# Optimization experiments

Measured on AMD Instinct MI355X. Metric: run time of the kernel, lower is better.

The kernel has to match this reference:

```python
import jax, jax.numpy as jnp
import numpy as np

D = 2048      # hidden
H = 16        # heads
HD = 128      # head dim
E = 64        # experts
K = 8         # top-k
F = 1024      # expert intermediate
B, S = 1, 256
EPS = 1e-05
THETA = 10000.0
SCALE = 0.08838834764831845  # 1/sqrt(128)


def _rms(x, w):
    return x * jax.lax.rsqrt(jnp.mean(x * x, axis=-1, keepdims=True) + EPS) * w


def _rotate_half(x):
    h = x.shape[-1] // 2
    return jnp.concatenate([-x[..., h:], x[..., :h]], axis=-1)


def setup_inputs() -> dict:
    key = jax.random.key(0)
    ks = jax.random.split(key, 16)
    std = 0.02
    return {
        "x": jax.random.normal(ks[0], (B, S, D), jnp.float32),
        "ln1_w": jnp.ones((D,), jnp.float32),
        "q_w": jax.random.normal(ks[1], (D, D), jnp.float32) * std,
        "k_w": jax.random.normal(ks[2], (D, D), jnp.float32) * std,
        "v_w": jax.random.normal(ks[3], (D, D), jnp.float32) * std,
        "o_w": jax.random.normal(ks[4], (D, D), jnp.float32) * std,
        "qn_w": jnp.ones((D,), jnp.float32),
        "kn_w": jnp.ones((D,), jnp.float32),
        "ln2_w": jnp.ones((D,), jnp.float32),
        "router_w": jax.random.normal(ks[5], (E, D), jnp.float32) * std,
        "gate_w": jax.random.normal(ks[6], (E, F, D), jnp.float32) * std,
        "up_w": jax.random.normal(ks[7], (E, F, D), jnp.float32) * std,
        "down_w": jax.random.normal(ks[8], (E, D, F), jnp.float32) * std,
    }


def reference(x, ln1_w, q_w, k_w, v_w, o_w, qn_w, kn_w, ln2_w,
              router_w, gate_w, up_w, down_w):
    b, s, d = x.shape
    # ---- attention ----
    xn = _rms(x, ln1_w)
    q = _rms(jnp.einsum('bsd,od->bso', xn, q_w), qn_w)
    k = _rms(jnp.einsum('bsd,od->bso', xn, k_w), kn_w)
    v = jnp.einsum('bsd,od->bso', xn, v_w)
    q = q.reshape(b, s, H, HD).transpose(0, 2, 1, 3)  # [b,h,s,hd]
    k = k.reshape(b, s, H, HD).transpose(0, 2, 1, 3)
    v = v.reshape(b, s, H, HD).transpose(0, 2, 1, 3)
    # RoPE
    inv_freq = 1.0 / (THETA ** (jnp.arange(0, HD, 2, dtype=jnp.float32) / HD))
    ang = jnp.arange(s, dtype=jnp.float32)[:, None] * inv_freq[None, :]  # [s, hd/2]
    emb = jnp.concatenate([ang, ang], axis=-1)
    cos, sin = jnp.cos(emb).astype(x.dtype), jnp.sin(emb).astype(x.dtype)
    q = q * cos + _rotate_half(q) * sin
    k = k * cos + _rotate_half(k) * sin
    scores = jnp.einsum('bhqd,bhkd->bhqk', q, k) * SCALE
    causal = jnp.tril(jnp.ones((s, s), bool))
    scores = jnp.where(causal, scores, jnp.finfo(scores.dtype).min)
    attn = jax.nn.softmax(scores, axis=-1)
    ctx = jnp.einsum('bhqk,bhkd->bhqd', attn, v)
    ctx = ctx.transpose(0, 2, 1, 3).reshape(b, s, d)
    h = x + jnp.einsum('bsd,od->bso', ctx, o_w)
    # ---- MoE ----
    hn = _rms(h, ln2_w)
    logits = jnp.einsum('bsd,ed->bse', hn, router_w)
    probs = jax.nn.softmax(logits.astype(jnp.float32), axis=-1)
    vals, idx = jax.lax.top_k(probs, K)  # [b,s,K]
    # dense combine weights [b,s,E]; OLMoE does not renormalize top-k probs
    combine = jnp.sum(jax.nn.one_hot(idx, E, dtype=jnp.float32) * vals[..., None], axis=-2)
    combine = combine.reshape(-1, E).astype(x.dtype)  # [T,E]
    xf = hn.reshape(-1, d)                            # [T,D]
    g = jnp.einsum('td,efd->etf', xf, gate_w)         # [E,T,F]
    u = jnp.einsum('td,efd->etf', xf, up_w)
    mid = jax.nn.silu(g) * u
    eo = jnp.einsum('etf,edf->etd', mid, down_w)      # [E,T,D]
    y = jnp.einsum('te,etd->td', combine, eo).reshape(b, s, d)
    return h + y
```

## Files before the change

### kernel.cpp

```cpp
#include <hip/hip_runtime.h>
#include <math.h>

#define DHID 2048
#define TOK 256
#define NHEAD 16
#define HDIM 128
#define NEXP 64
#define KSEL 8
#define FFD 1024
#define RMSEPS 1e-5f
#define ATTNSCALE 0.08838834764831845f

typedef short bf16x8 __attribute__((ext_vector_type(8)));
typedef float f32x4 __attribute__((ext_vector_type(4)));
typedef float f4 __attribute__((ext_vector_type(4)));

__device__ __forceinline__ unsigned short f2bf(float f){
  union { float f; unsigned int u; } c; c.f = f;
  unsigned int u = c.u + 0x7fffu + ((c.u>>16)&1u);
  return (unsigned short)(u>>16);
}
__device__ __forceinline__ unsigned int pk2(float a, float b){
  return (unsigned int)f2bf(a) | ((unsigned int)f2bf(b)<<16);
}
__device__ __forceinline__ bf16x8 as_bf8(uint4 u){
  union { uint4 u; bf16x8 v; } c; c.u = u; return c.v;
}

#define WAITV(N) { asm volatile("s_waitcnt vmcnt(" #N ")" ::: "memory"); __builtin_amdgcn_sched_barrier(0); }
#define WAITL0   { asm volatile("s_waitcnt lgkmcnt(0)" ::: "memory"); __builtin_amdgcn_sched_barrier(0); }
#define SB       __builtin_amdgcn_sched_barrier(0);

__global__ __launch_bounds__(256) void rms_kernel(const float* __restrict__ x,
    const float* __restrict__ w, unsigned short* __restrict__ obf,
    float* __restrict__ of32)
{
  int row = blockIdx.x, tid = threadIdx.x;
  const float* xr = x + (size_t)row*DHID;
  float4 a = *(const float4*)(xr + tid*8);
  float4 b = *(const float4*)(xr + tid*8 + 4);
  float ss = a.x*a.x+a.y*a.y+a.z*a.z+a.w*a.w + b.x*b.x+b.y*b.y+b.z*b.z+b.w*b.w;
  #pragma unroll
  for(int o=32;o>0;o>>=1) ss += __shfl_down(ss,o);
  __shared__ float red[4];
  if((tid&63)==0) red[tid>>6]=ss;
  __syncthreads();
  float r = rsqrtf((red[0]+red[1]+red[2]+red[3])*(1.0f/DHID) + RMSEPS);
  float v[8] = {a.x,a.y,a.z,a.w,b.x,b.y,b.z,b.w};
  unsigned short ob[8];
  #pragma unroll
  for(int j=0;j<8;j++){
    float val = v[j]*r*w[tid*8+j];
    ob[j]=f2bf(val);
    if(of32) of32[(size_t)row*DHID + tid*8 + j] = val;
  }
  uint4 o4;
  o4.x = (unsigned int)ob[0] | ((unsigned int)ob[1]<<16);
  o4.y = (unsigned int)ob[2] | ((unsigned int)ob[3]<<16);
  o4.z = (unsigned int)ob[4] | ((unsigned int)ob[5]<<16);
  o4.w = (unsigned int)ob[6] | ((unsigned int)ob[7]<<16);
  *(uint4*)(obf + (size_t)row*DHID + tid*8) = o4;
}

__global__ void rope_table_kernel(float* __restrict__ cs, float* __restrict__ sn){
  int i = blockIdx.x*256 + threadIdx.x;
  int s = i>>6, j = i&63;
  float invf = powf(10000.0f, -(float)j*(1.0f/64.0f));
  float ang = (float)s * invf;
  cs[i] = cosf(ang); sn[i] = sinf(ang);
}

__global__ __launch_bounds__(256) void gemm_qkv_kernel(
    const unsigned short* __restrict__ A,
    const float* __restrict__ qw, const float* __restrict__ kw, const float* __restrict__ vw,
    float* __restrict__ qo, float* __restrict__ ko, float* __restrict__ vo)
{
  int nt = blockIdx.x, mt = blockIdx.y;
  int which = nt>>5, nb = nt&31;
  const float* W = (which==0)? qw : (which==1)? kw : vw;
  float* OUT = (which==0)? qo : (which==1)? ko : vo;
  int n0 = nb*64, m0 = mt*64;
  __shared__ unsigned short As[64*64];
  __shared__ unsigned short Bs[64*64];
  int tid = threadIdx.x;
  int wid = tid>>6, lane = tid&63;
  int wm = wid>>1, wn = wid&1;
  int lr = lane&15, lg = lane>>4;
  int sr = tid>>2, sq = tid&3;
  f32x4 acc[2][2] = {};
  const unsigned short* Ap = A + (size_t)(m0+sr)*DHID + sq*16;
  const float* Bp = W + (size_t)(n0+sr)*DHID + sq*16;
  for(int k0=0;k0<DHID;k0+=64){
    uint4 a0 = *(const uint4*)(Ap + k0);
    uint4 a1 = *(const uint4*)(Ap + k0 + 8);
    float4 b0 = *(const float4*)(Bp + k0);
    float4 b1 = *(const float4*)(Bp + k0 + 4);
    float4 b2 = *(const float4*)(Bp + k0 + 8);
    float4 b3 = *(const float4*)(Bp + k0 + 12);
    int x7 = sr&7;
    *(uint4*)&As[sr*64 + (((sq*2)  ^ x7)*8)] = a0;
    *(uint4*)&As[sr*64 + (((sq*2+1)^ x7)*8)] = a1;
    uint4 p0 = make_uint4(pk2(b0.x,b0.y),pk2(b0.z,b0.w),pk2(b1.x,b1.y),pk2(b1.z,b1.w));
    uint4 p1 = make_uint4(pk2(b2.x,b2.y),pk2(b2.z,b2.w),pk2(b3.x,b3.y),pk2(b3.z,b3.w));
    *(uint4*)&Bs[sr*64 + (((sq*2)  ^ x7)*8)] = p0;
    *(uint4*)&Bs[sr*64 + (((sq*2+1)^ x7)*8)] = p1;
    __syncthreads();
    #pragma unroll
    for(int ki=0;ki<2;ki++){
      bf16x8 af[2], bfr[2];
      #pragma unroll
      for(int mi=0;mi<2;mi++){
        int r = wm*32 + mi*16 + lr;
        af[mi] = *(const bf16x8*)&As[r*64 + (((ki*4+lg)^(r&7))*8)];
      }
      #pragma unroll
      for(int ni=0;ni<2;ni++){
        int r = wn*32 + ni*16 + lr;
        bfr[ni] = *(const bf16x8*)&Bs[r*64 + (((ki*4+lg)^(r&7))*8)];
      }
      #pragma unroll
      for(int mi=0;mi<2;mi++)
        #pragma unroll
        for(int ni=0;ni<2;ni++)
          acc[mi][ni] = __builtin_amdgcn_mfma_f32_16x16x32_bf16(af[mi], bfr[ni], acc[mi][ni], 0,0,0);
    }
    __syncthreads();
  }
  #pragma unroll
  for(int mi=0;mi<2;mi++){
    #pragma unroll
    for(int ni=0;ni<2;ni++){
      int col = n0 + wn*32 + ni*16 + lr;
      int rowb = m0 + wm*32 + mi*16 + lg*4;
      #pragma unroll
      for(int rg=0;rg<4;rg++)
        OUT[(size_t)(rowb+rg)*DHID + col] = acc[mi][ni][rg];
    }
  }
}

__global__ __launch_bounds__(256) void gemm_o_kernel(const float* __restrict__ A,
  const float* __restrict__ W, const float* __restrict__ X,
  float* __restrict__ H, float* __restrict__ O)
{
  int nb = blockIdx.x, mt = blockIdx.y;
  int n0 = nb*64, m0 = mt*64;
  __shared__ unsigned short As[64*64];
  __shared__ unsigned short Bs[64*64];
  int tid = threadIdx.x;
  int wid = tid>>6, lane = tid&63;
  int wm = wid>>1, wn = wid&1;
  int lr = lane&15, lg = lane>>4;
  int sr = tid>>2, sq = tid&3;
  f32x4 acc[2][2] = {};
  const float* Ap = A + (size_t)(m0+sr)*DHID + sq*16;
  const float* Bp = W + (size_t)(n0+sr)*DHID + sq*16;
  for(int k0=0;k0<DHID;k0+=64){
    float4 a0=*(const float4*)(Ap+k0),   a1=*(const float4*)(Ap+k0+4);
    float4 a2=*(const float4*)(Ap+k0+8), a3=*(const float4*)(Ap+k0+12);
    float4 b0=*(const float4*)(Bp+k0),   b1=*(const float4*)(Bp+k0+4);
    float4 b2=*(const float4*)(Bp+k0+8), b3=*(const float4*)(Bp+k0+12);
    int x7 = sr&7;
    uint4 pa0 = make_uint4(pk2(a0.x,a0.y),pk2(a0.z,a0.w),pk2(a1.x,a1.y),pk2(a1.z,a1.w));
    uint4 pa1 = make_uint4(pk2(a2.x,a2.y),pk2(a2.z,a2.w),pk2(a3.x,a3.y),pk2(a3.z,a3.w));
    uint4 pb0 = make_uint4(pk2(b0.x,b0.y),pk2(b0.z,b0.w),pk2(b1.x,b1.y),pk2(b1.z,b1.w));
    uint4 pb1 = make_uint4(pk2(b2.x,b2.y),pk2(b2.z,b2.w),pk2(b3.x,b3.y),pk2(b3.z,b3.w));
    *(uint4*)&As[sr*64 + (((sq*2)  ^ x7)*8)] = pa0;
    *(uint4*)&As[sr*64 + (((sq*2+1)^ x7)*8)] = pa1;
    *(uint4*)&Bs[sr*64 + (((sq*2)  ^ x7)*8)] = pb0;
    *(uint4*)&Bs[sr*64 + (((sq*2+1)^ x7)*8)] = pb1;
    __syncthreads();
    #pragma unroll
    for(int ki=0;ki<2;ki++){
      bf16x8 af[2], bfr[2];
      #pragma unroll
      for(int mi=0;mi<2;mi++){
        int r = wm*32 + mi*16 + lr;
        af[mi] = *(const bf16x8*)&As[r*64 + (((ki*4+lg)^(r&7))*8)];
      }
      #pragma unroll
      for(int ni=0;ni<2;ni++){
        int r = wn*32 + ni*16 + lr;
        bfr[ni] = *(const bf16x8*)&Bs[r*64 + (((ki*4+lg)^(r&7))*8)];
      }
      #pragma unroll
      for(int mi=0;mi<2;mi++)
        #pragma unroll
        for(int ni=0;ni<2;ni++)
          acc[mi][ni] = __builtin_amdgcn_mfma_f32_16x16x32_bf16(af[mi], bfr[ni], acc[mi][ni], 0,0,0);
    }
    __syncthreads();
  }
  #pragma unroll
  for(int mi=0;mi<2;mi++){
    #pragma unroll
    for(int ni=0;ni<2;ni++){
      int col = n0 + wn*32 + ni*16 + lr;
      int rowb = m0 + wm*32 + mi*16 + lg*4;
      #pragma unroll
      for(int rg=0;rg<4;rg++){
        size_t idx = (size_t)(rowb+rg)*DHID + col;
        float v = acc[mi][ni][rg] + X[idx];
        H[idx] = v; O[idx] = v;
      }
    }
  }
}

__global__ __launch_bounds__(256) void qknorm_rope_kernel(const float* __restrict__ in,
   const float* __restrict__ w, const float* __restrict__ cs, const float* __restrict__ sn,
   float* __restrict__ out)
{
  int t = blockIdx.x, tid = threadIdx.x;
  __shared__ float xs[DHID];
  const float* xr = in + (size_t)t*DHID;
  float4 a = *(const float4*)(xr + tid*8);
  float4 b = *(const float4*)(xr + tid*8 + 4);
  *(float4*)&xs[tid*8] = a; *(float4*)&xs[tid*8+4] = b;
  float ss = a.x*a.x+a.y*a.y+a.z*a.z+a.w*a.w + b.x*b.x+b.y*b.y+b.z*b.z+b.w*b.w;
  #pragma unroll
  for(int o=32;o>0;o>>=1) ss += __shfl_down(ss,o);
  __shared__ float red[4];
  if((tid&63)==0) red[tid>>6]=ss;
  __syncthreads();
  float r = rsqrtf((red[0]+red[1]+red[2]+red[3])*(1.0f/DHID) + RMSEPS);
  int hh = tid>>4, jb = (tid&15)*4;
  #pragma unroll
  for(int p=0;p<4;p++){
    int j = jb+p;
    int i0 = hh*HDIM + j, i1 = i0+64;
    float va = xs[i0]*r*w[i0];
    float vb = xs[i1]*r*w[i1];
    float c = cs[t*64+j], s = sn[t*64+j];
    out[((size_t)(hh*TOK + t))*HDIM + j]    = va*c - vb*s;
    out[((size_t)(hh*TOK + t))*HDIM + j+64] = vb*c + va*s;
  }
}

__global__ __launch_bounds__(256) void attn_kernel(const float* __restrict__ qh,
  const float* __restrict__ kh, const float* __restrict__ vf, float* __restrict__ ctx)
{
  int head = blockIdx.x>>4, qt = blockIdx.x&15;
  __shared__ float qs[16][132];
  __shared__ float sc[16][260];
  __shared__ float red[16][16];
  __shared__ float rmx[16], rsm[16];
  int tid = threadIdx.x;
  {
    int r = tid>>4, c = (tid&15)*8;
    const float* src = qh + ((size_t)(head*TOK + qt*16 + r))*HDIM + c;
    *(float4*)&qs[r][c]   = *(const float4*)(src);
    *(float4*)&qs[r][c+4] = *(const float4*)(src+4);
  }
  __syncthreads();
  int qi = tid&15, kk = tid>>4;
  int qg = qt*16 + qi;
  for(int k=kk; k<=qg; k+=16){
    const float* kp = kh + ((size_t)(head*TOK + k))*HDIM;
    float d = 0.f;
    #pragma unroll 8
    for(int c=0;c<128;c+=4){
      float4 kv = *(const float4*)(kp + c);
      float4 qv = *(const float4*)&qs[qi][c];
      d += qv.x*kv.x + qv.y*kv.y + qv.z*kv.z + qv.w*kv.w;
    }
    sc[qi][k] = d*ATTNSCALE;
  }
  float m = -1e30f;
  for(int k=kk;k<=qg;k+=16) m = fmaxf(m, sc[qi][k]);
  red[qi][kk] = m;
  __syncthreads();
  if(kk==0){
    float mm=-1e30f;
    #pragma unroll
    for(int j=0;j<16;j++) mm = fmaxf(mm, red[qi][j]);
    rmx[qi]=mm;
  }
  __syncthreads();
  float mm = rmx[qi];
  float s = 0.f;
  for(int k=kk;k<=qg;k+=16){ float pp = expf(sc[qi][k]-mm); sc[qi][k]=pp; s+=pp; }
  red[qi][kk]=s;
  __syncthreads();
  if(kk==0){
    float t_=0.f;
    #pragma unroll
    for(int j=0;j<16;j++) t_ += red[qi][j];
    rsm[qi]=t_;
  }
  __syncthreads();
  int dg = kk;
  float acc[8]={0,0,0,0,0,0,0,0};
  const float* vp = vf + head*HDIM + dg*8;
  for(int k=0;k<=qg;k++){
    float p = sc[qi][k];
    float4 v0 = *(const float4*)(vp + (size_t)k*DHID);
    float4 v1 = *(const float4*)(vp + (size_t)k*DHID + 4);
    acc[0]+=p*v0.x; acc[1]+=p*v0.y; acc[2]+=p*v0.z; acc[3]+=p*v0.w;
    acc[4]+=p*v1.x; acc[5]+=p*v1.y; acc[6]+=p*v1.z; acc[7]+=p*v1.w;
  }
  float inv = 1.0f/rsm[qi];
  float* op = ctx + ((size_t)(qt*16+qi))*DHID + head*HDIM + dg*8;
  *(float4*)(op)   = make_float4(acc[0]*inv, acc[1]*inv, acc[2]*inv, acc[3]*inv);
  *(float4*)(op+4) = make_float4(acc[4]*inv, acc[5]*inv, acc[6]*inv, acc[7]*inv);
}

__global__ __launch_bounds__(256) void router_kernel(const float* __restrict__ hn,
    const float* __restrict__ rw, int* __restrict__ counts, int* __restrict__ toklist,
    float* __restrict__ wlist)
{
  int t = blockIdx.x, tid = threadIdx.x;
  __shared__ float xs[DHID];
  __shared__ float part[NEXP*4];
  __shared__ float probs[NEXP];
  *(float4*)&xs[tid*8]   = *(const float4*)(hn + (size_t)t*DHID + tid*8);
  *(float4*)&xs[tid*8+4] = *(const float4*)(hn + (size_t)t*DHID + tid*8+4);
  __syncthreads();
  int e = tid&63, c = tid>>6;
  const float* w = rw + (size_t)e*DHID + c*512;
  const float* xc = xs + c*512;
  float d = 0.f;
  for(int i=0;i<512;i+=4){
    float4 wv = *(const float4*)(w+i);
    d += xc[i]*wv.x + xc[i+1]*wv.y + xc[i+2]*wv.z + xc[i+3]*wv.w;
  }
  part[c*64 + e] = d;
  __syncthreads();
  if(tid<64){
    float logit = part[tid] + part[64+tid] + part[128+tid] + part[192+tid];
    float m = logit;
    #pragma unroll
    for(int o=32;o>0;o>>=1) m = fmaxf(m, __shfl_xor(m,o));
    float p = expf(logit - m);
    float s = p;
    #pragma unroll
    for(int o=32;o>0;o>>=1) s += __shfl_xor(s,o);
    probs[tid] = p/s;
  }
  __syncthreads();
  if(tid==0){
    unsigned long long used = 0ull;
    for(int r=0;r<KSEL;r++){
      float best = -1.f; int bi = 0;
      for(int j=0;j<NEXP;j++){
        if(!((used>>j)&1ull) && probs[j]>best){ best=probs[j]; bi=j; }
      }
      used |= (1ull<<bi);
      int slot = atomicAdd(&counts[bi],1);
      toklist[bi*TOK+slot] = t;
      wlist[bi*TOK+slot] = best;
    }
  }
}

__global__ __launch_bounds__(256,2) void moe_gateup_kernel(const unsigned short* __restrict__ hnb,
  const float* __restrict__ gw, const float* __restrict__ uw,
  const int* __restrict__ counts,
  const int* __restrict__ toklist, const float* __restrict__ wlist,
  unsigned short* __restrict__ mid)
{
  int fb = blockIdx.x, e = blockIdx.y, mc = blockIdx.z;
  int cnt = counts[e];
  if(mc*128 >= cnt) return;
  int tid = threadIdx.x;
  __shared__ int sbase;
  if(tid<64){
    int c = counts[tid];
    int v = c;
    #pragma unroll
    for(int o=1;o<64;o<<=1){ int n=__shfl_up(v,o); if(tid>=o) v+=n; }
    if(tid==e) sbase = v - c;
  }
  __shared__ unsigned short Gs[64*256];
  __shared__ unsigned short Us[64*256];
  int w = tid>>6, lane = tid&63;
  int wm = w>>1, wn = w&1, lr = lane&15, lg = lane>>4;
  int mbase = mc*128 + wm*64;

  int r0 = w*16;
  const float* Gp = gw + ((size_t)e*FFD + fb*64 + r0)*DHID + lane*4;
  const float* Up = uw + ((size_t)e*FFD + fb*64 + r0)*DHID + lane*4;
  const unsigned short* Ap[4];
  #pragma unroll
  for(int mi=0;mi<4;mi++){
    int slot = mbase + mi*16 + lr;
    int acl = (slot<cnt)? slot : (cnt-1);
    Ap[mi] = hnb + (size_t)toklist[e*TOK+acl]*DHID + lg*8;
  }
  __syncthreads();
  int base = sbase;

  f32x4 ag[4][2]={}, au[4][2]={};
  f4 P[8], Q[8];
  int wu = lane>>1, wh = (lane&1)*4;

  #define ISSUE(BK,SRC,s,jb) { \
    _Pragma("unroll") \
    for(int j=0;j<8;j++) BK[j] = __builtin_nontemporal_load((const f4*)(SRC + (size_t)((jb)+j)*DHID + (s)*256)); }
  #define WRITE(BK,DST,jb) { \
    _Pragma("unroll") \
    for(int j=0;j<8;j++){ \
      int r = r0 + (jb) + j; \
      int p = (wu & ~15) | ((wu&15) ^ (r&15)); \
      uint2 val; val.x = pk2(BK[j][0],BK[j][1]); val.y = pk2(BK[j][2],BK[j][3]); \
      *(uint2*)&DST[r*256 + p*8 + wh] = val; } }
  #define COMPUTE(s) { \
    _Pragma("unroll") \
    for(int mi=0;mi<4;mi++){ \
      if(mbase + mi*16 < cnt){ \
        uint4 av[8]; \
        _Pragma("unroll") \
        for(int kf=0;kf<8;kf++) av[kf] = *(const uint4*)(Ap[mi] + (size_t)(s)*256 + kf*32); \
        _Pragma("unroll") \
        for(int kf=0;kf<8;kf++){ \
          bf16x8 af = as_bf8(av[kf]); \
          _Pragma("unroll") \
          for(int ni=0;ni<2;ni++){ \
            int R = wn*32 + ni*16 + lr; \
            int v = kf*4 + lg; \
            int vp = (v & ~15) | ((v&15) ^ (R&15)); \
            int ho = R*256 + vp*8; \
            bf16x8 gfr = *(const bf16x8*)&Gs[ho]; \
            bf16x8 ufr = *(const bf16x8*)&Us[ho]; \
            ag[mi][ni] = __builtin_amdgcn_mfma_f32_16x16x32_bf16(af, gfr, ag[mi][ni], 0,0,0); \
            au[mi][ni] = __builtin_amdgcn_mfma_f32_16x16x32_bf16(af, ufr, au[mi][ni], 0,0,0); \
          } \
        } \
      } \
    } }

  const int NS = DHID/256;
  ISSUE(P, Gp, 0, 0)
  ISSUE(Q, Gp, 0, 8)
  for(int s=0;s<NS;s++){
    WAITV(8)
    WRITE(P, Gs, 0)
    ISSUE(P, Up, s, 0)
    WAITV(8)
    WRITE(Q, Gs, 8)
    ISSUE(Q, Up, s, 8)
    WAITV(8)
    WRITE(P, Us, 0)
    if(s+1<NS){ ISSUE(P, Gp, s+1, 0) }
    if(s+1<NS){ WAITV(8) } else { WAITV(0) }
    WRITE(Q, Us, 8)
    if(s+1<NS){ ISSUE(Q, Gp, s+1, 8) }
    WAITL0
    __builtin_amdgcn_s_barrier(); SB
    COMPUTE(s)
    __builtin_amdgcn_s_barrier(); SB
  }
  #undef ISSUE
  #undef WRITE
  #undef COMPUTE

  #pragma unroll
  for(int mi=0;mi<4;mi++){
    #pragma unroll
    for(int ni=0;ni<2;ni++){
      int f = fb*64 + wn*32 + ni*16 + lr;
      #pragma unroll
      for(int rg=0;rg<4;rg++){
        int slot = mbase + mi*16 + lg*4 + rg;
        if(slot < cnt){
          float cw = wlist[e*TOK + slot];
          float g = ag[mi][ni][rg], u = au[mi][ni][rg];
          float mval = g/(1.0f+expf(-g))*u*cw;
          mid[((size_t)(base+slot))*FFD + f] = f2bf(mval);
        }
      }
    }
  }
}

__global__ __launch_bounds__(256,4) void moe_down_kernel(const unsigned short* __restrict__ mid,
  const float* __restrict__ dwn, const int* __restrict__ counts,
  const int* __restrict__ toklist, float* __restrict__ out)
{
  int nb=blockIdx.x, e=blockIdx.y, mc=blockIdx.z;
  int cnt=counts[e];
  if(mc*128>=cnt) return;
  int tid=threadIdx.x;
  __shared__ int sbase;
  if(tid<64){
    int c = counts[tid];
    int v = c;
    #pragma unroll
    for(int o=1;o<64;o<<=1){ int n=__shfl_up(v,o); if(tid>=o) v+=n; }
    if(tid==e) sbase = v - c;
  }
  __shared__ unsigned short Ds[64*256];
  int w=tid>>6, lane=tid&63;
  int wm=w>>1, wn=w&1, lr=lane&15, lg=lane>>4;
  int mbase = mc*128 + wm*64;
  int r0 = w*16;
  const float* Dp = dwn + ((size_t)e*DHID + nb*64 + r0)*FFD + lane*4;
  __syncthreads();
  int base = sbase;
  const unsigned short* Ap[4];
  #pragma unroll
  for(int mi=0;mi<4;mi++){
    int slot = mbase + mi*16 + lr;
    int acl = (slot<cnt)? slot : (cnt-1);
    Ap[mi] = mid + (size_t)(base+acl)*FFD + lg*8;
  }

  f32x4 acc[4][2]={};
  f4 P[8], Q[8];
  int wu = lane>>1, wh = (lane&1)*4;

  #define ISSUE(BK,s,jb) { \
    _Pragma("unroll") \
    for(int j=0;j<8;j++) BK[j] = __builtin_nontemporal_load((const f4*)(Dp + (size_t)((jb)+j)*FFD + (s)*256)); }
  #define WRITE(BK,jb) { \
    _Pragma("unroll") \
    for(int j=0;j<8;j++){ \
      int r = r0 + (jb) + j; \
      int p = (wu & ~15) | ((wu&15) ^ (r&15)); \
      uint2 val; val.x = pk2(BK[j][0],BK[j][1]); val.y = pk2(BK[j][2],BK[j][3]); \
      *(uint2*)&Ds[r*256 + p*8 + wh] = val; } }
  #define COMPUTE(s) { \
    _Pragma("unroll") \
    for(int mi=0;mi<4;mi++){ \
      if(mbase + mi*16 < cnt){ \
        uint4 av[8]; \
        _Pragma("unroll") \
        for(int kf=0;kf<8;kf++) av[kf] = *(const uint4*)(Ap[mi] + (size_t)(s)*256 + kf*32); \
        _Pragma("unroll") \
        for(int kf=0;kf<8;kf++){ \
          bf16x8 af = as_bf8(av[kf]); \
          _Pragma("unroll") \
          for(int ni=0;ni<2;ni++){ \
            int R = wn*32 + ni*16 + lr; \
            int v = kf*4 + lg; \
            int vp = (v & ~15) | ((v&15) ^ (R&15)); \
            bf16x8 dfr = *(const bf16x8*)&Ds[R*256 + vp*8]; \
            acc[mi][ni] = __builtin_amdgcn_mfma_f32_16x16x32_bf16(af, dfr, acc[mi][ni], 0,0,0); \
          } \
        } \
      } \
    } }

  const int NS = FFD/256;
  ISSUE(P, 0, 0)
  ISSUE(Q, 0, 8)
  for(int s=0;s<NS;s++){
    WAITV(8)
    WRITE(P, 0)
    if(s+1<NS){ ISSUE(P, s+1, 0) }
    if(s+1<NS){ WAITV(8) } else { WAITV(0) }
    WRITE(Q, 8)
    if(s+1<NS){ ISSUE(Q, s+1, 8) }
    WAITL0
    __builtin_amdgcn_s_barrier(); SB
    COMPUTE(s)
    __builtin_amdgcn_s_barrier(); SB
  }
  #undef ISSUE
  #undef WRITE
  #undef COMPUTE

  #pragma unroll
  for(int mi=0;mi<4;mi++){
    #pragma unroll
    for(int ni=0;ni<2;ni++){
      int d = nb*64 + wn*32 + ni*16 + lr;
      #pragma unroll
      for(int rg=0;rg<4;rg++){
        int slot = mbase + mi*16 + lg*4 + rg;
        if(slot<cnt){
          int tok = toklist[e*TOK + slot];
          atomicAdd(out + (size_t)tok*DHID + d, acc[mi][ni][rg]);
        }
      }
    }
  }
}

extern "C" void kernel_launch(void* const* d_in, const int* in_sizes, int n_in,
                              void* d_out, int out_size, void* d_ws, size_t ws_size,
                              hipStream_t stream)
{
  (void)in_sizes; (void)n_in; (void)out_size; (void)ws_size;
  const float* x    = (const float*)d_in[0];
  const float* ln1w = (const float*)d_in[1];
  const float* qw   = (const float*)d_in[2];
  const float* kw   = (const float*)d_in[3];
  const float* vw   = (const float*)d_in[4];
  const float* ow   = (const float*)d_in[5];
  const float* qnw  = (const float*)d_in[6];
  const float* knw  = (const float*)d_in[7];
  const float* ln2w = (const float*)d_in[8];
  const float* rw   = (const float*)d_in[9];
  const float* gw   = (const float*)d_in[10];
  const float* uw   = (const float*)d_in[11];
  const float* dwn  = (const float*)d_in[12];
  float* out = (float*)d_out;

  char* p = (char*)d_ws;
  auto alloc = [&](size_t bytes)->void*{ void* r = (void*)p; p += (bytes + 255) & ~(size_t)255; return r; };
  unsigned short* xnb = (unsigned short*)alloc((size_t)TOK*DHID*2);
  float* qf   = (float*)alloc((size_t)TOK*DHID*4);
  float* kf   = (float*)alloc((size_t)TOK*DHID*4);
  float* vf   = (float*)alloc((size_t)TOK*DHID*4);
  float* qh   = (float*)alloc((size_t)TOK*DHID*4);
  float* kh   = (float*)alloc((size_t)TOK*DHID*4);
  float* ctx  = (float*)alloc((size_t)TOK*DHID*4);
  float* hbuf = (float*)alloc((size_t)TOK*DHID*4);
  float* hnf  = (float*)alloc((size_t)TOK*DHID*4);
  unsigned short* hnb = (unsigned short*)alloc((size_t)TOK*DHID*2);
  float* csb  = (float*)alloc((size_t)TOK*64*4);
  float* snb  = (float*)alloc((size_t)TOK*64*4);
  int* counts = (int*)alloc(NEXP*4);
  int* toklist= (int*)alloc((size_t)NEXP*TOK*4);
  float* wlist= (float*)alloc((size_t)NEXP*TOK*4);
  unsigned short* mid = (unsigned short*)alloc((size_t)TOK*KSEL*FFD*2);

  rope_table_kernel<<<64,256,0,stream>>>(csb,snb);
  rms_kernel<<<TOK,256,0,stream>>>(x, ln1w, xnb, nullptr);
  gemm_qkv_kernel<<<dim3(96,4),256,0,stream>>>(xnb,qw,kw,vw,qf,kf,vf);
  qknorm_rope_kernel<<<TOK,256,0,stream>>>(qf,qnw,csb,snb,qh);
  qknorm_rope_kernel<<<TOK,256,0,stream>>>(kf,knw,csb,snb,kh);
  attn_kernel<<<256,256,0,stream>>>(qh,kh,vf,ctx);
  gemm_o_kernel<<<dim3(32,4),256,0,stream>>>(ctx,ow,x,hbuf,out);
  rms_kernel<<<TOK,256,0,stream>>>(hbuf, ln2w, hnb, hnf);
  hipMemsetAsync(counts,0,NEXP*4,stream);
  router_kernel<<<TOK,256,0,stream>>>(hnf,rw,counts,toklist,wlist);
  moe_gateup_kernel<<<dim3(16,NEXP,2),256,0,stream>>>(hnb,gw,uw,counts,toklist,wlist,mid);
  moe_down_kernel<<<dim3(32,NEXP,2),256,0,stream>>>(mid,dwn,counts,toklist,out);
}
```

Baseline: 584.6 us.

## Halve MoE token tile, deepen weight prefetch, and prefetch activations across stages

Both MoE expert kernels now use a 64-token tile instead of 128 and launch 4 token chunks. Gate/up gains two more register buffers so the gate and up weights for the next K-stage are all in flight at once, and the activation fragments for the next stage are loaded during the current stage's compute. The down kernel gets the same activation prefetch, with its launch-bound occupancy hint lowered to 2. The aim is to overlap the fp32 weight streaming better with compute and use more blocks when expert counts are small. The cost is higher register pressure and re-streaming weights for every extra token chunk, since each expert's weights are now read once per 64 tokens rather than once per 128.

```diff
diff --git a/kernel.cpp b/kernel.cpp
--- a/kernel.cpp
+++ b/kernel.cpp
@@ -361,7 +361,7 @@
 {
   int fb = blockIdx.x, e = blockIdx.y, mc = blockIdx.z;
   int cnt = counts[e];
-  if(mc*128 >= cnt) return;
+  if(mc*64 >= cnt) return;
   int tid = threadIdx.x;
   __shared__ int sbase;
   if(tid<64){
@@ -375,14 +375,14 @@
   __shared__ unsigned short Us[64*256];
   int w = tid>>6, lane = tid&63;
   int wm = w>>1, wn = w&1, lr = lane&15, lg = lane>>4;
-  int mbase = mc*128 + wm*64;
+  int mbase = mc*64 + wm*32;
 
   int r0 = w*16;
   const float* Gp = gw + ((size_t)e*FFD + fb*64 + r0)*DHID + lane*4;
   const float* Up = uw + ((size_t)e*FFD + fb*64 + r0)*DHID + lane*4;
-  const unsigned short* Ap[4];
-  #pragma unroll
-  for(int mi=0;mi<4;mi++){
+  const unsigned short* Ap[2];
+  #pragma unroll
+  for(int mi=0;mi<2;mi++){
     int slot = mbase + mi*16 + lr;
     int acl = (slot<cnt)? slot : (cnt-1);
     Ap[mi] = hnb + (size_t)toklist[e*TOK+acl]*DHID + lg*8;
@@ -390,8 +390,9 @@
   __syncthreads();
   int base = sbase;
 
-  f32x4 ag[4][2]={}, au[4][2]={};
-  f4 P[8], Q[8];
+  f32x4 ag[2][2]={}, au[2][2]={};
+  f4 P[8], Q[8], R[8], S[8];
+  uint4 av[2][8];
   int wu = lane>>1, wh = (lane&1)*4;
 
   #define ISSUE(BK,SRC,s,jb) { \
@@ -404,22 +405,24 @@
       int p = (wu & ~15) | ((wu&15) ^ (r&15)); \
       uint2 val; val.x = pk2(BK[j][0],BK[j][1]); val.y = pk2(BK[j][2],BK[j][3]); \
       *(uint2*)&DST[r*256 + p*8 + wh] = val; } }
-  #define COMPUTE(s) { \
-    _Pragma("unroll") \
-    for(int mi=0;mi<4;mi++){ \
+  #define ISSUE_A(s) { \
+    _Pragma("unroll") \
+    for(int mi=0;mi<2;mi++) \
+      _Pragma("unroll") \
+      for(int kf=0;kf<8;kf++) av[mi][kf] = *(const uint4*)(Ap[mi] + (size_t)(s)*256 + kf*32); }
+  #define COMPUTE() { \
+    _Pragma("unroll") \
+    for(int mi=0;mi<2;mi++){ \
       if(mbase + mi*16 < cnt){ \
-        uint4 av[8]; \
-        _Pragma("unroll") \
-        for(int kf=0;kf<8;kf++) av[kf] = *(const uint4*)(Ap[mi] + (size_t)(s)*256 + kf*32); \
         _Pragma("unroll") \
         for(int kf=0;kf<8;kf++){ \
-          bf16x8 af = as_bf8(av[kf]); \
+          bf16x8 af = as_bf8(av[mi][kf]); \
           _Pragma("unroll") \
           for(int ni=0;ni<2;ni++){ \
-            int R = wn*32 + ni*16 + lr; \
+            int Rr = wn*32 + ni*16 + lr; \
             int v = kf*4 + lg; \
-            int vp = (v & ~15) | ((v&15) ^ (R&15)); \
-            int ho = R*256 + vp*8; \
+            int vp = (v & ~15) | ((v&15) ^ (Rr&15)); \
+            int ho = Rr*256 + vp*8; \
             bf16x8 gfr = *(const bf16x8*)&Gs[ho]; \
             bf16x8 ufr = *(const bf16x8*)&Us[ho]; \
             ag[mi][ni] = __builtin_amdgcn_mfma_f32_16x16x32_bf16(af, gfr, ag[mi][ni], 0,0,0); \
@@ -432,30 +435,52 @@
   const int NS = DHID/256;
   ISSUE(P, Gp, 0, 0)
   ISSUE(Q, Gp, 0, 8)
+  ISSUE(R, Up, 0, 0)
+  ISSUE(S, Up, 0, 8)
+  ISSUE_A(0)
   for(int s=0;s<NS;s++){
-    WAITV(8)
-    WRITE(P, Gs, 0)
-    ISSUE(P, Up, s, 0)
-    WAITV(8)
-    WRITE(Q, Gs, 8)
-    ISSUE(Q, Up, s, 8)
-    WAITV(8)
-    WRITE(P, Us, 0)
-    if(s+1<NS){ ISSUE(P, Gp, s+1, 0) }
-    if(s+1<NS){ WAITV(8) } else { WAITV(0) }
-    WRITE(Q, Us, 8)
-    if(s+1<NS){ ISSUE(Q, Gp, s+1, 8) }
-    WAITL0
-    __builtin_amdgcn_s_barrier(); SB
-    COMPUTE(s)
-    __builtin_amdgcn_s_barrier(); SB
+    if(s+1<NS){
+      WAITV(40)
+      WRITE(P, Gs, 0)
+      ISSUE(P, Gp, s+1, 0)
+      WAITV(40)
+      WRITE(Q, Gs, 8)
+      ISSUE(Q, Gp, s+1, 8)
+      WAITV(40)
+      WRITE(R, Us, 0)
+      ISSUE(R, Up, s+1, 0)
+      WAITV(40)
+      WRITE(S, Us, 8)
+      ISSUE(S, Up, s+1, 8)
+      WAITV(32)
+      WAITL0
+      __builtin_amdgcn_s_barrier(); SB
+      COMPUTE()
+      ISSUE_A(s+1)
+      __builtin_amdgcn_s_barrier(); SB
+    } else {
+      WAITV(40)
+      WRITE(P, Gs, 0)
+      WAITV(32)
+      WRITE(Q, Gs, 8)
+      WAITV(24)
+      WRITE(R, Us, 0)
+      WAITV(16)
+      WRITE(S, Us, 8)
+      WAITV(0)
+      WAITL0
+      __builtin_amdgcn_s_barrier(); SB
+      COMPUTE()
+      __builtin_amdgcn_s_barrier(); SB
+    }
   }
   #undef ISSUE
   #undef WRITE
+  #undef ISSUE_A
   #undef COMPUTE
 
   #pragma unroll
-  for(int mi=0;mi<4;mi++){
+  for(int mi=0;mi<2;mi++){
     #pragma unroll
     for(int ni=0;ni<2;ni++){
       int f = fb*64 + wn*32 + ni*16 + lr;
@@ -473,13 +498,13 @@
   }
 }
 
-__global__ __launch_bounds__(256,4) void moe_down_kernel(const unsigned short* __restrict__ mid,
+__global__ __launch_bounds__(256,2) void moe_down_kernel(const unsigned short* __restrict__ mid,
   const float* __restrict__ dwn, const int* __restrict__ counts,
   const int* __restrict__ toklist, float* __restrict__ out)
 {
   int nb=blockIdx.x, e=blockIdx.y, mc=blockIdx.z;
   int cnt=counts[e];
-  if(mc*128>=cnt) return;
+  if(mc*64>=cnt) return;
   int tid=threadIdx.x;
   __shared__ int sbase;
   if(tid<64){
@@ -492,21 +517,22 @@
   __shared__ unsigned short Ds[64*256];
   int w=tid>>6, lane=tid&63;
   int wm=w>>1, wn=w&1, lr=lane&15, lg=lane>>4;
-  int mbase = mc*128 + wm*64;
+  int mbase = mc*64 + wm*32;
   int r0 = w*16;
   const float* Dp = dwn + ((size_t)e*DHID + nb*64 + r0)*FFD + lane*4;
   __syncthreads();
   int base = sbase;
-  const unsigned short* Ap[4];
-  #pragma unroll
-  for(int mi=0;mi<4;mi++){
+  const unsigned short* Ap[2];
+  #pragma unroll
+  for(int mi=0;mi<2;mi++){
     int slot = mbase + mi*16 + lr;
     int acl = (slot<cnt)? slot : (cnt-1);
     Ap[mi] = mid + (size_t)(base+acl)*FFD + lg*8;
   }
 
-  f32x4 acc[4][2]={};
+  f32x4 acc[2][2]={};
   f4 P[8], Q[8];
+  uint4 av[2][8];
   int wu = lane>>1, wh = (lane&1)*4;
 
   #define ISSUE(BK,s,jb) { \
@@ -519,22 +545,24 @@
       int p = (wu & ~15) | ((wu&15) ^ (r&15)); \
       uint2 val; val.x = pk2(BK[j][0],BK[j][1]); val.y = pk2(BK[j][2],BK[j][3]); \
       *(uint2*)&Ds[r*256 + p*8 + wh] = val; } }
-  #define COMPUTE(s) { \
-    _Pragma("unroll") \
-    for(int mi=0;mi<4;mi++){ \
+  #define ISSUE_A(s) { \
+    _Pragma("unroll") \
+    for(int mi=0;mi<2;mi++) \
+      _Pragma("unroll") \
+      for(int kf=0;kf<8;kf++) av[mi][kf] = *(const uint4*)(Ap[mi] + (size_t)(s)*256 + kf*32); }
+  #define COMPUTE() { \
+    _Pragma("unroll") \
+    for(int mi=0;mi<2;mi++){ \
       if(mbase + mi*16 < cnt){ \
-        uint4 av[8]; \
-        _Pragma("unroll") \
-        for(int kf=0;kf<8;kf++) av[kf] = *(const uint4*)(Ap[mi] + (size_t)(s)*256 + kf*32); \
         _Pragma("unroll") \
         for(int kf=0;kf<8;kf++){ \
-          bf16x8 af = as_bf8(av[kf]); \
+          bf16x8 af = as_bf8(av[mi][kf]); \
           _Pragma("unroll") \
           for(int ni=0;ni<2;ni++){ \
-            int R = wn*32 + ni*16 + lr; \
+            int Rr = wn*32 + ni*16 + lr; \
             int v = kf*4 + lg; \
-            int vp = (v & ~15) | ((v&15) ^ (R&15)); \
-            bf16x8 dfr = *(const bf16x8*)&Ds[R*256 + vp*8]; \
+            int vp = (v & ~15) | ((v&15) ^ (Rr&15)); \
+            bf16x8 dfr = *(const bf16x8*)&Ds[Rr*256 + vp*8]; \
             acc[mi][ni] = __builtin_amdgcn_mfma_f32_16x16x32_bf16(af, dfr, acc[mi][ni], 0,0,0); \
           } \
         } \
@@ -544,24 +572,38 @@
   const int NS = FFD/256;
   ISSUE(P, 0, 0)
   ISSUE(Q, 0, 8)
+  ISSUE_A(0)
   for(int s=0;s<NS;s++){
-    WAITV(8)
-    WRITE(P, 0)
-    if(s+1<NS){ ISSUE(P, s+1, 0) }
-    if(s+1<NS){ WAITV(8) } else { WAITV(0) }
-    WRITE(Q, 8)
-    if(s+1<NS){ ISSUE(Q, s+1, 8) }
-    WAITL0
-    __builtin_amdgcn_s_barrier(); SB
-    COMPUTE(s)
-    __builtin_amdgcn_s_barrier(); SB
+    if(s+1<NS){
+      WAITV(24)
+      WRITE(P, 0)
+      ISSUE(P, s+1, 0)
+      WAITV(8)
+      WRITE(Q, 8)
+      ISSUE(Q, s+1, 8)
+      WAITL0
+      __builtin_amdgcn_s_barrier(); SB
+      COMPUTE()
+      ISSUE_A(s+1)
+      __builtin_amdgcn_s_barrier(); SB
+    } else {
+      WAITV(24)
+      WRITE(P, 0)
+      WAITV(0)
+      WRITE(Q, 8)
+      WAITL0
+      __builtin_amdgcn_s_barrier(); SB
+      COMPUTE()
+      __builtin_amdgcn_s_barrier(); SB
+    }
   }
   #undef ISSUE
   #undef WRITE
+  #undef ISSUE_A
   #undef COMPUTE
 
   #pragma unroll
-  for(int mi=0;mi<4;mi++){
+  for(int mi=0;mi<2;mi++){
     #pragma unroll
     for(int ni=0;ni<2;ni++){
       int d = nb*64 + wn*32 + ni*16 + lr;
@@ -626,6 +668,6 @@
   rms_kernel<<<TOK,256,0,stream>>>(hbuf, ln2w, hnb, hnf);
   hipMemsetAsync(counts,0,NEXP*4,stream);
   router_kernel<<<TOK,256,0,stream>>>(hnf,rw,counts,toklist,wlist);
-  moe_gateup_kernel<<<dim3(16,NEXP,2),256,0,stream>>>(hnb,gw,uw,counts,toklist,wlist,mid);
-  moe_down_kernel<<<dim3(32,NEXP,2),256,0,stream>>>(mid,dwn,counts,toklist,out);
-}
+  moe_gateup_kernel<<<dim3(16,NEXP,4),256,0,stream>>>(hnb,gw,uw,counts,toklist,wlist,mid);
+  moe_down_kernel<<<dim3(32,NEXP,4),256,0,stream>>>(mid,dwn,counts,toklist,out);
+}
```

Result: slower. 1.627 ms (+178.2%).
